# Performance work log

Hardware: AMD Instinct MI355X
Metric: run time of the kernel (lower is better)

The kernel has to match this reference:

```python
import jax, jax.numpy as jnp
import numpy as np

N_NODES = 50000

def _gat_conv(x, src, dst, W, a_src, a_dst, bias, num_nodes, concat, neg_slope=0.2):
    # x: [N, Fin]; W: [Fin, H*C]; a_src/a_dst: [H, C]; src/dst: [E]
    H, C = a_src.shape
    h = (x @ W).reshape(-1, H, C)                      # [N, H, C]
    alpha_s = jnp.einsum('nhc,hc->nh', h, a_src)        # [N, H]
    alpha_d = jnp.einsum('nhc,hc->nh', h, a_dst)        # [N, H]
    e = alpha_s[src] + alpha_d[dst]                     # [E, H]
    e = jax.nn.leaky_relu(e, neg_slope)
    # segment softmax over destination nodes
    m = jax.ops.segment_max(e, dst, num_segments=num_nodes)   # [N, H]
    ex = jnp.exp(e - m[dst])                                   # [E, H]
    denom = jax.ops.segment_sum(ex, dst, num_segments=num_nodes)  # [N, H]
    alpha = ex / denom[dst]                                    # [E, H]
    msg = h[src] * alpha[:, :, None]                            # [E, H, C]
    out = jax.ops.segment_sum(msg, dst, num_segments=num_nodes)  # [N, H, C]
    if concat:
        out = out.reshape(-1, H * C)
    else:
        out = out.mean(axis=1)
    return out + bias

def _add_self_loops(edge_index, num_nodes):
    loop = jnp.arange(num_nodes, dtype=edge_index.dtype)
    src = jnp.concatenate([edge_index[0], loop])
    dst = jnp.concatenate([edge_index[1], loop])
    return src, dst

def setup_inputs() -> dict:
    key = jax.random.key(0)
    ks = jax.random.split(key, 12)
    N, E = N_NODES, 800000
    in_c, hid, out_c, H = 128, 32, 64, 4
    x = jax.random.normal(ks[0], (N, in_c), dtype=jnp.float32)
    edge_index = jax.random.randint(ks[1], (2, E), 0, N, dtype=jnp.int64)
    edge_weight = jax.random.uniform(ks[2], (E,), dtype=jnp.float32)
    s1 = 1.0 / np.sqrt(in_c)
    s2 = 1.0 / np.sqrt(hid * H)
    W1 = jax.random.normal(ks[3], (in_c, H * hid), dtype=jnp.float32) * s1
    a_src1 = jax.random.normal(ks[4], (H, hid), dtype=jnp.float32) * s1
    a_dst1 = jax.random.normal(ks[5], (H, hid), dtype=jnp.float32) * s1
    b1 = jnp.zeros((H * hid,), dtype=jnp.float32)
    W2 = jax.random.normal(ks[6], (H * hid, out_c), dtype=jnp.float32) * s2
    a_src2 = jax.random.normal(ks[7], (1, out_c), dtype=jnp.float32) * s2
    a_dst2 = jax.random.normal(ks[8], (1, out_c), dtype=jnp.float32) * s2
    b2 = jnp.zeros((out_c,), dtype=jnp.float32)
    return {"x": x, "edge_index": edge_index, "edge_weight": edge_weight,
            "W1": W1, "a_src1": a_src1, "a_dst1": a_dst1, "b1": b1,
            "W2": W2, "a_src2": a_src2, "a_dst2": a_dst2, "b2": b2}

def reference(x, edge_index, edge_weight, W1, a_src1, a_dst1, b1, W2, a_src2, a_dst2, b2):
    # PyG GATConv with edge_dim unset ignores edge_weight; self-loops added by default
    N = x.shape[0]
    src, dst = _add_self_loops(edge_index, N)
    h = _gat_conv(x, src, dst, W1, a_src1, a_dst1, b1, N, concat=True)
    h = jax.nn.relu(h)
    out = _gat_conv(h, src, dst, W2, a_src2, a_dst2, b2, N, concat=False)
    return out
```

## Files before the change

kernel.cpp:

```cpp
#include <hip/hip_runtime.h>
#include <hip/hip_fp16.h>
#include <math.h>


#define NEG_SLOPE 0.2f
#define NBLKA 256
#define MAXNB 512
#define LDH 136

typedef _Float16 f16x8 __attribute__((ext_vector_type(8)));
typedef float f32x4 __attribute__((ext_vector_type(4)));

__device__ __forceinline__ float leaky(float v) { return v > 0.f ? v : NEG_SLOPE * v; }

__global__ __launch_bounds__(256) void histc_k(const int* __restrict__ ei, int E, int ET,
                                               int* __restrict__ blkpref, int NB,
                                               const float* __restrict__ W1,
                                               const float* __restrict__ W2,
                                               _Float16* __restrict__ w1t,
                                               _Float16* __restrict__ w2t) {
  __shared__ int lhist[MAXNB];
  int chunk = (ET + NBLKA - 1) / NBLKA;
  int e0 = blockIdx.x * chunk, e1 = min(ET, e0 + chunk);
  for (int b = threadIdx.x; b < NB; b += 256) lhist[b] = 0;
  __syncthreads();
  for (int e = e0 + threadIdx.x; e < e1; e += 256) {
    int d = (e < E) ? ei[E + e] : (e - E);
    atomicAdd(&lhist[d >> 7], 1);
  }
  __syncthreads();
  for (int b = threadIdx.x; b < NB; b += 256)
    blkpref[b * NBLKA + blockIdx.x] = lhist[b];
  if (blockIdx.x == 0) {
    int t = threadIdx.x;
    if (t < 128) {
      union { _Float16 h[8]; uint4 u; } buf;
      for (int k0 = 0; k0 < 128; k0 += 8) {
        #pragma unroll
        for (int u = 0; u < 8; ++u) buf.h[u] = (_Float16)W1[(k0 + u) * 128 + t];
        *(uint4*)&w1t[t * 128 + k0] = buf.u;
      }
    } else if (t < 192) {
      int n = t - 128;
      union { _Float16 h[8]; uint4 u; } buf;
      for (int k0 = 0; k0 < 128; k0 += 8) {
        #pragma unroll
        for (int u = 0; u < 8; ++u) buf.h[u] = (_Float16)W2[(k0 + u) * 64 + n];
        *(uint4*)&w2t[n * 128 + k0] = buf.u;
      }
    }
  }
}

__global__ __launch_bounds__(256) void scan_blk_k(int* __restrict__ blkpref,
                                                  int* __restrict__ bbase) {
  __shared__ int sm[NBLKA];
  int b = blockIdx.x, t = threadIdx.x;
  int v = blkpref[b * NBLKA + t];
  sm[t] = v;
  __syncthreads();
  #pragma unroll
  for (int off = 1; off < NBLKA; off <<= 1) {
    int x = (t >= off) ? sm[t - off] : 0;
    __syncthreads();
    sm[t] += x;
    __syncthreads();
  }
  blkpref[b * NBLKA + t] = sm[t] - v;
  if (t == NBLKA - 1) bbase[b] = sm[t];
}

__global__ __launch_bounds__(512) void scan_bkt_k(int* __restrict__ bbase,
                                                  int* __restrict__ lcnt,
                                                  int* __restrict__ rowptr,
                                                  int NB, int N, int ET) {
  __shared__ int sm[512];
  int t = threadIdx.x;
  int v = (t < NB) ? bbase[t] : 0;
  sm[t] = v;
  __syncthreads();
  #pragma unroll
  for (int off = 1; off < 512; off <<= 1) {
    int x = (t >= off) ? sm[t - off] : 0;
    __syncthreads();
    sm[t] += x;
    __syncthreads();
  }
  int excl = sm[t] - v;
  if (t <= NB) bbase[t] = excl;
  if (t == 0) { lcnt[0] = 0; lcnt[16] = 0; rowptr[N] = ET; }
}

__global__ __launch_bounds__(256) void passA_k(const int* __restrict__ ei, int E, int ET,
                                               const int* __restrict__ bbase,
                                               const int* __restrict__ blkpref,
                                               int* __restrict__ pairs, int NB) {
  __shared__ int lcur[MAXNB];
  int chunk = (ET + NBLKA - 1) / NBLKA;
  int e0 = blockIdx.x * chunk, e1 = min(ET, e0 + chunk);
  for (int b = threadIdx.x; b < NB; b += 256)
    lcur[b] = bbase[b] + blkpref[b * NBLKA + blockIdx.x];
  __syncthreads();
  for (int e = e0 + threadIdx.x; e < e1; e += 256) {
    int s, d;
    if (e < E) { s = ei[e]; d = ei[E + e]; } else { s = d = e - E; }
    int b = d >> 7;
    int pos = atomicAdd(&lcur[b], 1);
    pairs[pos] = ((d & 127) << 17) | s;
  }
}

__global__ __launch_bounds__(256) void passB_k(const int* __restrict__ pairs,
                                               const int* __restrict__ bbase,
                                               int* __restrict__ rowptr,
                                               int* __restrict__ srcs,
                                               int* __restrict__ small_list,
                                               int* __restrict__ big_list,
                                               int* __restrict__ lcnt, int N) {
  __shared__ int ncnt[128], spre[128], lcur[128];
  __shared__ int wcS[2], wcB[2], bS, bB;
  int b = blockIdx.x, t = threadIdx.x;
  int nb0 = b << 7;
  int nn = min(128, N - nb0);
  int e0 = bbase[b], e1 = bbase[b + 1];
  if (t < 128) ncnt[t] = 0;
  __syncthreads();
  for (int r = e0 + t; r < e1; r += 256)
    atomicAdd(&ncnt[pairs[r] >> 17], 1);
  __syncthreads();
  if (t < 128) spre[t] = ncnt[t];
  __syncthreads();
  #pragma unroll
  for (int off = 1; off < 128; off <<= 1) {
    int x = (t < 128 && t >= off) ? spre[t - off] : 0;
    __syncthreads();
    if (t < 128) spre[t] += x;
    __syncthreads();
  }
  if (t < nn) {
    int base = e0 + spre[t] - ncnt[t];
    rowptr[nb0 + t] = base;
    lcur[t] = base;
  }
  __syncthreads();
  for (int r = e0 + t; r < e1; r += 256) {
    int p = pairs[r];
    int pos = atomicAdd(&lcur[p >> 17], 1);
    srcs[pos] = p & 0x1FFFF;
  }
  int lane = t & 63, wv = t >> 6;
  bool valid = (t < nn);
  int deg = valid ? ncnt[t] : 0;
  bool isS = valid && (deg <= 16);
  bool isB = valid && (deg > 16);
  unsigned long long ms = __ballot(isS);
  unsigned long long mb = __ballot(isB);
  if (lane == 0 && wv < 2) { wcS[wv] = __popcll(ms); wcB[wv] = __popcll(mb); }
  __syncthreads();
  if (t == 0) {
    bS = atomicAdd(&lcnt[0],  wcS[0] + wcS[1]);
    bB = atomicAdd(&lcnt[16], wcB[0] + wcB[1]);
  }
  __syncthreads();
  unsigned long long below = (lane == 0) ? 0ull : (~0ull >> (64 - lane));
  int offS = bS + ((wv == 1) ? wcS[0] : 0);
  int offB = bB + ((wv == 1) ? wcB[0] : 0);
  if (isS) small_list[offS + __popcll(ms & below)] = nb0 + t;
  if (isB) big_list[offB + __popcll(mb & below)]   = nb0 + t;
}

__global__ __launch_bounds__(256) void gemm1_k(const float* __restrict__ X,
                                               const _Float16* __restrict__ WT,
                                               const float* __restrict__ aw_s,
                                               const float* __restrict__ aw_d,
                                               __half* __restrict__ Hh,
                                               float* __restrict__ as,
                                               float* __restrict__ ad, int N) {
  __shared__ _Float16 xs[64 * LDH];
  __shared__ _Float16 wt[128 * LDH];
  int t = threadIdx.x;
  int n0 = blockIdx.x * 64;
  for (int i = t; i < 2048; i += 256) {
    int r = i >> 4, c8 = i & 15;
    *(uint4*)&wt[r * LDH + c8 * 8] = ((const uint4*)WT)[i];
  }
  for (int i = t; i < 2048; i += 256) {
    int r = i >> 5, c4 = i & 31;
    int n = n0 + r;
    float4 xv = (n < N) ? ((const float4*)X)[(size_t)n * 32 + c4]
                        : make_float4(0.f, 0.f, 0.f, 0.f);
    __half2 h0 = __floats2half2_rn(xv.x, xv.y);
    __half2 h1 = __floats2half2_rn(xv.z, xv.w);
    uint2 u; u.x = *(unsigned*)&h0; u.y = *(unsigned*)&h1;
    *(uint2*)&xs[r * LDH + c4 * 4] = u;
  }
  __syncthreads();
  int wv = t >> 6, l = t & 63;
  int row16 = l & 15, kg = l >> 4;
  f32x4 acc[8];
  #pragma unroll
  for (int j = 0; j < 8; ++j) acc[j] = (f32x4){0.f, 0.f, 0.f, 0.f};
  #pragma unroll
  for (int kk = 0; kk < 4; ++kk) {
    int kbase = kk * 32 + kg * 8;
    f16x8 afr = *(f16x8*)&xs[(wv * 16 + row16) * LDH + kbase];
    #pragma unroll
    for (int j = 0; j < 8; ++j) {
      f16x8 bfr = *(f16x8*)&wt[(j * 16 + row16) * LDH + kbase];
      acc[j] = __builtin_amdgcn_mfma_f32_16x16x32_f16(afr, bfr, acc[j], 0, 0, 0);
    }
  }
  __syncthreads();
  #pragma unroll
  for (int j = 0; j < 8; ++j) {
    int col = j * 16 + row16;
    #pragma unroll
    for (int r = 0; r < 4; ++r) {
      int row = wv * 16 + kg * 4 + r;
      xs[row * LDH + col] = (_Float16)acc[j][r];
    }
  }
  __syncthreads();
  for (int i = t; i < 1024; i += 256) {
    int r = i >> 4, c8 = i & 15;
    int n = n0 + r;
    if (n < N) ((uint4*)Hh)[(size_t)n * 16 + c8] = *(uint4*)&xs[r * LDH + c8 * 8];
  }
  {
    int r = t >> 2, h = t & 3;
    int n = n0 + r;
    float ps = 0.f, pd = 0.f;
    #pragma unroll
    for (int q = 0; q < 4; ++q) {
      f16x8 hv = *(f16x8*)&xs[r * LDH + h * 32 + q * 8];
      float4 s0 = *(const float4*)&aw_s[h * 32 + q * 8];
      float4 s1 = *(const float4*)&aw_s[h * 32 + q * 8 + 4];
      float4 d0 = *(const float4*)&aw_d[h * 32 + q * 8];
      float4 d1 = *(const float4*)&aw_d[h * 32 + q * 8 + 4];
      ps += (float)hv[0] * s0.x + (float)hv[1] * s0.y + (float)hv[2] * s0.z + (float)hv[3] * s0.w
          + (float)hv[4] * s1.x + (float)hv[5] * s1.y + (float)hv[6] * s1.z + (float)hv[7] * s1.w;
      pd += (float)hv[0] * d0.x + (float)hv[1] * d0.y + (float)hv[2] * d0.z + (float)hv[3] * d0.w
          + (float)hv[4] * d1.x + (float)hv[5] * d1.y + (float)hv[6] * d1.z + (float)hv[7] * d1.w;
    }
    if (n < N) { as[n * 4 + h] = ps; ad[n * 4 + h] = pd; }
  }
}

__global__ __launch_bounds__(256) void gemm2_k(const __half* __restrict__ X,
                                               const _Float16* __restrict__ WT,
                                               const float* __restrict__ aw_s,
                                               const float* __restrict__ aw_d,
                                               __half* __restrict__ Hh,
                                               float* __restrict__ as,
                                               float* __restrict__ ad, int N) {
  __shared__ _Float16 xs[64 * LDH];
  __shared__ _Float16 wt[64 * LDH];
  int t = threadIdx.x;
  int n0 = blockIdx.x * 64;
  for (int i = t; i < 1024; i += 256) {
    int r = i >> 4, c8 = i & 15;
    *(uint4*)&wt[r * LDH + c8 * 8] = ((const uint4*)WT)[i];
  }
  for (int i = t; i < 1024; i += 256) {
    int r = i >> 4, c8 = i & 15;
    int n = n0 + r;
    uint4 v = (n < N) ? ((const uint4*)X)[(size_t)n * 16 + c8] : make_uint4(0, 0, 0, 0);
    *(uint4*)&xs[r * LDH + c8 * 8] = v;
  }
  __syncthreads();
  int wv = t >> 6, l = t & 63;
  int row16 = l & 15, kg = l >> 4;
  f32x4 acc[4];
  #pragma unroll
  for (int j = 0; j < 4; ++j) acc[j] = (f32x4){0.f, 0.f, 0.f, 0.f};
  #pragma unroll
  for (int kk = 0; kk < 4; ++kk) {
    int kbase = kk * 32 + kg * 8;
    f16x8 afr = *(f16x8*)&xs[(wv * 16 + row16) * LDH + kbase];
    #pragma unroll
    for (int j = 0; j < 4; ++j) {
      f16x8 bfr = *(f16x8*)&wt[(j * 16 + row16) * LDH + kbase];
      acc[j] = __builtin_amdgcn_mfma_f32_16x16x32_f16(afr, bfr, acc[j], 0, 0, 0);
    }
  }
  __syncthreads();
  #pragma unroll
  for (int j = 0; j < 4; ++j) {
    int col = j * 16 + row16;
    #pragma unroll
    for (int r = 0; r < 4; ++r) {
      int row = wv * 16 + kg * 4 + r;
      xs[row * LDH + col] = (_Float16)acc[j][r];
    }
  }
  __syncthreads();
  for (int i = t; i < 512; i += 256) {
    int r = i >> 3, c8 = i & 7;
    int n = n0 + r;
    if (n < N) ((uint4*)Hh)[(size_t)n * 8 + c8] = *(uint4*)&xs[r * LDH + c8 * 8];
  }
  {
    int r = t >> 2, q = t & 3;
    int n = n0 + r;
    float ps = 0.f, pd = 0.f;
    #pragma unroll
    for (int qq = 0; qq < 2; ++qq) {
      f16x8 hv = *(f16x8*)&xs[r * LDH + q * 16 + qq * 8];
      float4 s0 = *(const float4*)&aw_s[q * 16 + qq * 8];
      float4 s1 = *(const float4*)&aw_s[q * 16 + qq * 8 + 4];
      float4 d0 = *(const float4*)&aw_d[q * 16 + qq * 8];
      float4 d1 = *(const float4*)&aw_d[q * 16 + qq * 8 + 4];
      ps += (float)hv[0] * s0.x + (float)hv[1] * s0.y + (float)hv[2] * s0.z + (float)hv[3] * s0.w
          + (float)hv[4] * s1.x + (float)hv[5] * s1.y + (float)hv[6] * s1.z + (float)hv[7] * s1.w;
      pd += (float)hv[0] * d0.x + (float)hv[1] * d0.y + (float)hv[2] * d0.z + (float)hv[3] * d0.w
          + (float)hv[4] * d1.x + (float)hv[5] * d1.y + (float)hv[6] * d1.z + (float)hv[7] * d1.w;
    }
    ps += __shfl_xor(ps, 1); ps += __shfl_xor(ps, 2);
    pd += __shfl_xor(pd, 1); pd += __shfl_xor(pd, 2);
    if (q == 0 && n < N) { as[n] = ps; ad[n] = pd; }
  }
}

__device__ __forceinline__ void load8h(const __half* p, float* f) {
  uint4 hv = *(const uint4*)p;
  float2 f0 = __half22float2(*(const __half2*)&hv.x);
  float2 f1 = __half22float2(*(const __half2*)&hv.y);
  float2 f2 = __half22float2(*(const __half2*)&hv.z);
  float2 f3 = __half22float2(*(const __half2*)&hv.w);
  f[0] = f0.x; f[1] = f0.y; f[2] = f1.x; f[3] = f1.y;
  f[4] = f2.x; f[5] = f2.y; f[6] = f3.x; f[7] = f3.y;
}

__global__ __launch_bounds__(256) void agg1_k(const int* __restrict__ rowptr,
                                              const int* __restrict__ srcs,
                                              const float* __restrict__ as,
                                              const float* __restrict__ ad,
                                              const __half* __restrict__ Hm,
                                              const float* __restrict__ bias,
                                              __half* __restrict__ out,
                                              const int* __restrict__ small_list,
                                              const int* __restrict__ big_list,
                                              const int* __restrict__ lcnt, int SB) {
  if (blockIdx.x < (unsigned)SB) {
    __shared__ float al_sm[16][17][4];
    __shared__ int   sr_sm[16][16];
    int g  = threadIdx.x >> 4;
    int gl = threadIdx.x & 15;
    int gidx = blockIdx.x * 16 + g;
    if (gidx >= lcnt[0]) return;
    int n = small_list[gidx];
    int r0 = rowptr[n];
    int deg = rowptr[n + 1] - r0;
    float4 adn = *(const float4*)&ad[n * 4];

    float e0 = -INFINITY, e1 = -INFINITY, e2 = -INFINITY, e3 = -INFINITY;
    int s = 0;
    if (gl < deg) {
      s = srcs[r0 + gl];
      float4 av = *(const float4*)&as[s * 4];
      e0 = leaky(av.x + adn.x); e1 = leaky(av.y + adn.y);
      e2 = leaky(av.z + adn.z); e3 = leaky(av.w + adn.w);
    }
    sr_sm[g][gl] = s;
    float m0 = e0, m1 = e1, m2 = e2, m3 = e3;
    #pragma unroll
    for (int off = 8; off > 0; off >>= 1) {
      m0 = fmaxf(m0, __shfl_xor(m0, off, 16)); m1 = fmaxf(m1, __shfl_xor(m1, off, 16));
      m2 = fmaxf(m2, __shfl_xor(m2, off, 16)); m3 = fmaxf(m3, __shfl_xor(m3, off, 16));
    }
    float sc0 = (gl < deg) ? __expf(e0 - m0) : 0.f;
    float sc1 = (gl < deg) ? __expf(e1 - m1) : 0.f;
    float sc2 = (gl < deg) ? __expf(e2 - m2) : 0.f;
    float sc3 = (gl < deg) ? __expf(e3 - m3) : 0.f;
    float s0 = sc0, s1 = sc1, s2 = sc2, s3 = sc3;
    #pragma unroll
    for (int off = 8; off > 0; off >>= 1) {
      s0 += __shfl_xor(s0, off, 16); s1 += __shfl_xor(s1, off, 16);
      s2 += __shfl_xor(s2, off, 16); s3 += __shfl_xor(s3, off, 16);
    }
    *(float4*)&al_sm[g][gl][0] =
        make_float4(sc0 / s0, sc1 / s1, sc2 / s2, sc3 / s3);

    int h = gl >> 2;
    int cbase = gl * 8;
    float a0 = 0.f, a1 = 0.f, a2 = 0.f, a3 = 0.f,
          a4 = 0.f, a5 = 0.f, a6 = 0.f, a7 = 0.f;
    for (int j = 0; j < deg; j += 4) {
      #pragma unroll
      for (int u = 0; u < 4; ++u) {
        int idx = j + u;
        bool vU = idx < deg;
        int jj = vU ? idx : 0;
        int   sU  = sr_sm[g][jj];
        float alU = vU ? al_sm[g][jj][h] : 0.f;
        float f[8];
        load8h(&Hm[(size_t)sU * 128 + cbase], f);
        a0 += f[0] * alU; a1 += f[1] * alU; a2 += f[2] * alU; a3 += f[3] * alU;
        a4 += f[4] * alU; a5 += f[5] * alU; a6 += f[6] * alU; a7 += f[7] * alU;
      }
    }
    float4 b0 = *(const float4*)&bias[cbase];
    float4 b1 = *(const float4*)&bias[cbase + 4];
    __half2* dst = (__half2*)&out[(size_t)n * 128 + cbase];
    dst[0] = __floats2half2_rn(fmaxf(a0 + b0.x, 0.f), fmaxf(a1 + b0.y, 0.f));
    dst[1] = __floats2half2_rn(fmaxf(a2 + b0.z, 0.f), fmaxf(a3 + b0.w, 0.f));
    dst[2] = __floats2half2_rn(fmaxf(a4 + b1.x, 0.f), fmaxf(a5 + b1.y, 0.f));
    dst[3] = __floats2half2_rn(fmaxf(a6 + b1.z, 0.f), fmaxf(a7 + b1.w, 0.f));
    return;
  }
  __shared__ float al_sm[4][64][4];
  __shared__ int   sr_sm[4][64];
  int wv = threadIdx.x >> 6, lane = threadIdx.x & 63;
  int widx = (blockIdx.x - SB) * 4 + wv;
  if (widx >= lcnt[16]) return;
  int n = big_list[widx];
  int r0 = rowptr[n], r1 = rowptr[n + 1];
  int deg = r1 - r0;
  int grp = lane >> 4, gl = lane & 15, h = gl >> 2;
  int cbase = gl * 8;
  float4 adn = *(const float4*)&ad[n * 4];

  float a0 = 0.f, a1 = 0.f, a2 = 0.f, a3 = 0.f,
        a4 = 0.f, a5 = 0.f, a6 = 0.f, a7 = 0.f;

  if (deg <= 64) {
    float e0 = -INFINITY, e1 = -INFINITY, e2 = -INFINITY, e3 = -INFINITY;
    int s = 0;
    if (lane < deg) {
      s = srcs[r0 + lane];
      float4 av = *(const float4*)&as[s * 4];
      e0 = leaky(av.x + adn.x); e1 = leaky(av.y + adn.y);
      e2 = leaky(av.z + adn.z); e3 = leaky(av.w + adn.w);
    }
    sr_sm[wv][lane] = s;
    float m0 = e0, m1 = e1, m2 = e2, m3 = e3;
    #pragma unroll
    for (int off = 32; off > 0; off >>= 1) {
      m0 = fmaxf(m0, __shfl_xor(m0, off)); m1 = fmaxf(m1, __shfl_xor(m1, off));
      m2 = fmaxf(m2, __shfl_xor(m2, off)); m3 = fmaxf(m3, __shfl_xor(m3, off));
    }
    float sc0 = (lane < deg) ? __expf(e0 - m0) : 0.f;
    float sc1 = (lane < deg) ? __expf(e1 - m1) : 0.f;
    float sc2 = (lane < deg) ? __expf(e2 - m2) : 0.f;
    float sc3 = (lane < deg) ? __expf(e3 - m3) : 0.f;
    float s0 = sc0, s1 = sc1, s2 = sc2, s3 = sc3;
    #pragma unroll
    for (int off = 32; off > 0; off >>= 1) {
      s0 += __shfl_xor(s0, off); s1 += __shfl_xor(s1, off);
      s2 += __shfl_xor(s2, off); s3 += __shfl_xor(s3, off);
    }
    *(float4*)&al_sm[wv][lane][0] =
        make_float4(sc0 / s0, sc1 / s1, sc2 / s2, sc3 / s3);

    for (int base = 0; base < deg; base += 16) {
      #pragma unroll
      for (int u = 0; u < 4; ++u) {
        int idx = base + grp * 4 + u;
        bool vU = idx < deg;
        int jj = vU ? idx : 0;
        int   sU  = sr_sm[wv][jj];
        float alU = vU ? al_sm[wv][jj][h] : 0.f;
        float f[8];
        load8h(&Hm[(size_t)sU * 128 + cbase], f);
        a0 += f[0] * alU; a1 += f[1] * alU; a2 += f[2] * alU; a3 += f[3] * alU;
        a4 += f[4] * alU; a5 += f[5] * alU; a6 += f[6] * alU; a7 += f[7] * alU;
      }
    }
  } else {
    float m0 = -INFINITY, m1 = -INFINITY, m2 = -INFINITY, m3 = -INFINITY;
    for (int r = r0 + lane; r < r1; r += 64) {
      int s = srcs[r];
      float4 av = *(const float4*)&as[s * 4];
      m0 = fmaxf(m0, leaky(av.x + adn.x)); m1 = fmaxf(m1, leaky(av.y + adn.y));
      m2 = fmaxf(m2, leaky(av.z + adn.z)); m3 = fmaxf(m3, leaky(av.w + adn.w));
    }
    #pragma unroll
    for (int off = 32; off > 0; off >>= 1) {
      m0 = fmaxf(m0, __shfl_xor(m0, off)); m1 = fmaxf(m1, __shfl_xor(m1, off));
      m2 = fmaxf(m2, __shfl_xor(m2, off)); m3 = fmaxf(m3, __shfl_xor(m3, off));
    }
    float s0 = 0.f, s1 = 0.f, s2 = 0.f, s3 = 0.f;
    for (int r = r0 + lane; r < r1; r += 64) {
      int s = srcs[r];
      float4 av = *(const float4*)&as[s * 4];
      s0 += __expf(leaky(av.x + adn.x) - m0); s1 += __expf(leaky(av.y + adn.y) - m1);
      s2 += __expf(leaky(av.z + adn.z) - m2); s3 += __expf(leaky(av.w + adn.w) - m3);
    }
    #pragma unroll
    for (int off = 32; off > 0; off >>= 1) {
      s0 += __shfl_xor(s0, off); s1 += __shfl_xor(s1, off);
      s2 += __shfl_xor(s2, off); s3 += __shfl_xor(s3, off);
    }
    float mhh = (h == 0) ? m0 : (h == 1) ? m1 : (h == 2) ? m2 : m3;
    float inv = 1.f / ((h == 0) ? s0 : (h == 1) ? s1 : (h == 2) ? s2 : s3);
    float adh = (h == 0) ? adn.x : (h == 1) ? adn.y : (h == 2) ? adn.z : adn.w;
    for (int r = r0; r < r1; r += 8) {
      int rA = r + grp, rB = rA + 4;
      bool vA = rA < r1, vB = rB < r1;
      int sA = srcs[vA ? rA : r0];
      int sB = srcs[vB ? rB : r0];
      float avA = as[sA * 4 + h], avB = as[sB * 4 + h];
      float alA = vA ? (__expf(leaky(avA + adh) - mhh) * inv) : 0.f;
      float alB = vB ? (__expf(leaky(avB + adh) - mhh) * inv) : 0.f;
      float fA[8], fB[8];
      load8h(&Hm[(size_t)sA * 128 + cbase], fA);
      load8h(&Hm[(size_t)sB * 128 + cbase], fB);
      a0 += fA[0] * alA + fB[0] * alB; a1 += fA[1] * alA + fB[1] * alB;
      a2 += fA[2] * alA + fB[2] * alB; a3 += fA[3] * alA + fB[3] * alB;
      a4 += fA[4] * alA + fB[4] * alB; a5 += fA[5] * alA + fB[5] * alB;
      a6 += fA[6] * alA + fB[6] * alB; a7 += fA[7] * alA + fB[7] * alB;
    }
  }
  a0 += __shfl_xor(a0, 16); a0 += __shfl_xor(a0, 32);
  a1 += __shfl_xor(a1, 16); a1 += __shfl_xor(a1, 32);
  a2 += __shfl_xor(a2, 16); a2 += __shfl_xor(a2, 32);
  a3 += __shfl_xor(a3, 16); a3 += __shfl_xor(a3, 32);
  a4 += __shfl_xor(a4, 16); a4 += __shfl_xor(a4, 32);
  a5 += __shfl_xor(a5, 16); a5 += __shfl_xor(a5, 32);
  a6 += __shfl_xor(a6, 16); a6 += __shfl_xor(a6, 32);
  a7 += __shfl_xor(a7, 16); a7 += __shfl_xor(a7, 32);
  if (grp == 0) {
    float4 b0 = *(const float4*)&bias[cbase];
    float4 b1 = *(const float4*)&bias[cbase + 4];
    __half2* dst = (__half2*)&out[(size_t)n * 128 + cbase];
    dst[0] = __floats2half2_rn(fmaxf(a0 + b0.x, 0.f), fmaxf(a1 + b0.y, 0.f));
    dst[1] = __floats2half2_rn(fmaxf(a2 + b0.z, 0.f), fmaxf(a3 + b0.w, 0.f));
    dst[2] = __floats2half2_rn(fmaxf(a4 + b1.x, 0.f), fmaxf(a5 + b1.y, 0.f));
    dst[3] = __floats2half2_rn(fmaxf(a6 + b1.z, 0.f), fmaxf(a7 + b1.w, 0.f));
  }
}

__global__ __launch_bounds__(256) void agg2_k(const int* __restrict__ rowptr,
                                              const int* __restrict__ srcs,
                                              const float* __restrict__ as,
                                              const float* __restrict__ ad,
                                              const __half* __restrict__ Hm,
                                              const float* __restrict__ bias,
                                              float* __restrict__ out,
                                              const int* __restrict__ small_list,
                                              const int* __restrict__ big_list,
                                              const int* __restrict__ lcnt, int SB) {
  if (blockIdx.x < (unsigned)SB) {
    __shared__ float al_sm[16][17];
    __shared__ int   sr_sm[16][16];
    int g  = threadIdx.x >> 4;
    int gl = threadIdx.x & 15;
    int gidx = blockIdx.x * 16 + g;
    if (gidx >= lcnt[0]) return;
    int n = small_list[gidx];
    int r0 = rowptr[n];
    int deg = rowptr[n + 1] - r0;
    float adn = ad[n];

    float e = -INFINITY;
    int s = 0;
    if (gl < deg) { s = srcs[r0 + gl]; e = leaky(as[s] + adn); }
    sr_sm[g][gl] = s;
    float m = e;
    #pragma unroll
    for (int off = 8; off > 0; off >>= 1) m = fmaxf(m, __shfl_xor(m, off, 16));
    float sc = (gl < deg) ? __expf(e - m) : 0.f;
    float ssum = sc;
    #pragma unroll
    for (int off = 8; off > 0; off >>= 1) ssum += __shfl_xor(ssum, off, 16);
    al_sm[g][gl] = sc / ssum;

    int cbase = gl * 4;
    float a0 = 0.f, a1 = 0.f, a2 = 0.f, a3 = 0.f;
    for (int j = 0; j < deg; j += 4) {
      #pragma unroll
      for (int u = 0; u < 4; ++u) {
        int idx = j + u;
        bool vU = idx < deg;
        int jj = vU ? idx : 0;
        int   sU  = sr_sm[g][jj];
        float alU = vU ? al_sm[g][jj] : 0.f;
        uint2 hv = *(const uint2*)&Hm[(size_t)sU * 64 + cbase];
        float2 f0 = __half22float2(*(const __half2*)&hv.x);
        float2 f1 = __half22float2(*(const __half2*)&hv.y);
        a0 += f0.x * alU; a1 += f0.y * alU; a2 += f1.x * alU; a3 += f1.y * alU;
      }
    }
    float4 bv = *(const float4*)&bias[cbase];
    float4 o;
    o.x = a0 + bv.x; o.y = a1 + bv.y; o.z = a2 + bv.z; o.w = a3 + bv.w;
    *(float4*)&out[(size_t)n * 64 + cbase] = o;
    return;
  }
  __shared__ float al_sm[4][64];
  __shared__ int   sr_sm[4][64];
  int wv = threadIdx.x >> 6, lane = threadIdx.x & 63;
  int widx = (blockIdx.x - SB) * 4 + wv;
  if (widx >= lcnt[16]) return;
  int n = big_list[widx];
  int r0 = rowptr[n], r1 = rowptr[n + 1];
  int deg = r1 - r0;
  int grp = lane >> 4, gl = lane & 15;
  int cbase = gl * 4;
  float adn = ad[n];

  float a0 = 0.f, a1 = 0.f, a2 = 0.f, a3 = 0.f;

  if (deg <= 64) {
    float e = -INFINITY;
    int s = 0;
    if (lane < deg) { s = srcs[r0 + lane]; e = leaky(as[s] + adn); }
    sr_sm[wv][lane] = s;
    float m = e;
    #pragma unroll
    for (int off = 32; off > 0; off >>= 1) m = fmaxf(m, __shfl_xor(m, off));
    float sc = (lane < deg) ? __expf(e - m) : 0.f;
    float ssum = sc;
    #pragma unroll
    for (int off = 32; off > 0; off >>= 1) ssum += __shfl_xor(ssum, off);
    al_sm[wv][lane] = sc / ssum;

    for (int base = 0; base < deg; base += 16) {
      #pragma unroll
      for (int u = 0; u < 4; ++u) {
        int idx = base + grp * 4 + u;
        bool vU = idx < deg;
        int jj = vU ? idx : 0;
        int   sU  = sr_sm[wv][jj];
        float alU = vU ? al_sm[wv][jj] : 0.f;
        uint2 hv = *(const uint2*)&Hm[(size_t)sU * 64 + cbase];
        float2 f0 = __half22float2(*(const __half2*)&hv.x);
        float2 f1 = __half22float2(*(const __half2*)&hv.y);
        a0 += f0.x * alU; a1 += f0.y * alU; a2 += f1.x * alU; a3 += f1.y * alU;
      }
    }
  } else {
    float mh = -INFINITY;
    for (int r = r0 + lane; r < r1; r += 64)
      mh = fmaxf(mh, leaky(as[srcs[r]] + adn));
    #pragma unroll
    for (int off = 32; off > 0; off >>= 1) mh = fmaxf(mh, __shfl_xor(mh, off));
    float ssum = 0.f;
    for (int r = r0 + lane; r < r1; r += 64)
      ssum += __expf(leaky(as[srcs[r]] + adn) - mh);
    #pragma unroll
    for (int off = 32; off > 0; off >>= 1) ssum += __shfl_xor(ssum, off);
    float inv = 1.f / ssum;
    for (int r = r0; r < r1; r += 8) {
      int rA = r + grp, rB = rA + 4;
      bool vA = rA < r1, vB = rB < r1;
      int sA = srcs[vA ? rA : r0];
      int sB = srcs[vB ? rB : r0];
      float alA = vA ? (__expf(leaky(as[sA] + adn) - mh) * inv) : 0.f;
      float alB = vB ? (__expf(leaky(as[sB] + adn) - mh) * inv) : 0.f;
      uint2 hvA = *(const uint2*)&Hm[(size_t)sA * 64 + cbase];
      uint2 hvB = *(const uint2*)&Hm[(size_t)sB * 64 + cbase];
      float2 fA0 = __half22float2(*(const __half2*)&hvA.x);
      float2 fA1 = __half22float2(*(const __half2*)&hvA.y);
      float2 fB0 = __half22float2(*(const __half2*)&hvB.x);
      float2 fB1 = __half22float2(*(const __half2*)&hvB.y);
      a0 += fA0.x * alA + fB0.x * alB; a1 += fA0.y * alA + fB0.y * alB;
      a2 += fA1.x * alA + fB1.x * alB; a3 += fA1.y * alA + fB1.y * alB;
    }
  }
  a0 += __shfl_xor(a0, 16); a0 += __shfl_xor(a0, 32);
  a1 += __shfl_xor(a1, 16); a1 += __shfl_xor(a1, 32);
  a2 += __shfl_xor(a2, 16); a2 += __shfl_xor(a2, 32);
  a3 += __shfl_xor(a3, 16); a3 += __shfl_xor(a3, 32);
  if (grp == 0) {
    float4 bv = *(const float4*)&bias[cbase];
    float4 o;
    o.x = a0 + bv.x; o.y = a1 + bv.y; o.z = a2 + bv.z; o.w = a3 + bv.w;
    *(float4*)&out[(size_t)n * 64 + cbase] = o;
  }
}

extern "C" void kernel_launch(void* const* d_in, const int* in_sizes, int n_in,
                              void* d_out, int out_size, void* d_ws, size_t ws_size,
                              hipStream_t stream) {
  const float* x   = (const float*)d_in[0];
  const int*   ei  = (const int*)d_in[1];
  const float* W1  = (const float*)d_in[3];
  const float* aS1 = (const float*)d_in[4];
  const float* aD1 = (const float*)d_in[5];
  const float* b1  = (const float*)d_in[6];
  const float* W2  = (const float*)d_in[7];
  const float* aS2 = (const float*)d_in[8];
  const float* aD2 = (const float*)d_in[9];
  const float* b2  = (const float*)d_in[10];

  const int N  = in_sizes[0] / 128;
  const int E  = in_sizes[2];
  const int ET = E + N;
  const int NB = (N + 127) >> 7;

  float* ws    = (float*)d_ws;
  __half* h1h  = (__half*)ws;
  __half* o1h  = (__half*)(ws + (size_t)N * 64);
  float* as1   = ws + (size_t)N * 128;
  float* ad1   = as1  + (size_t)4 * N;
  float* as2   = ad1  + (size_t)4 * N;
  float* ad2   = as2  + (size_t)N;
  int*   lcnt    = (int*)(ad2 + (size_t)N);
  int*   rowptr  = lcnt + 32;
  int*   bbase   = rowptr + N + 1;
  int*   blkpref = bbase + NB + 1;
  int*   small_list = blkpref + NB * NBLKA;
  int*   big_list   = small_list + N;
  int*   srcs   = big_list + N;
  _Float16* w1t = (_Float16*)(srcs + ET);
  _Float16* w2t = w1t + 128 * 128;
  int*   pairs  = (int*)ws;
  __half* h2h  = h1h;
  float* out  = (float*)d_out;

  const int gb = (N + 63) / 64;
  const int sb = (N + 15) / 16;
  const int bb = (N + 3) / 4;

  histc_k<<<NBLKA, 256, 0, stream>>>(ei, E, ET, blkpref, NB, W1, W2, w1t, w2t);
  scan_blk_k<<<NB, 256, 0, stream>>>(blkpref, bbase);
  scan_bkt_k<<<1, 512, 0, stream>>>(bbase, lcnt, rowptr, NB, N, ET);
  passA_k<<<NBLKA, 256, 0, stream>>>(ei, E, ET, bbase, blkpref, pairs, NB);
  passB_k<<<NB, 256, 0, stream>>>(pairs, bbase, rowptr, srcs,
                                  small_list, big_list, lcnt, N);

  gemm1_k<<<gb, 256, 0, stream>>>(x, w1t, aS1, aD1, h1h, as1, ad1, N);
  agg1_k<<<sb + bb, 256, 0, stream>>>(rowptr, srcs, as1, ad1, h1h, b1, o1h,
                                      small_list, big_list, lcnt, sb);

  gemm2_k<<<gb, 256, 0, stream>>>(o1h, w2t, aS2, aD2, h2h, as2, ad2, N);
  agg2_k<<<sb + bb, 256, 0, stream>>>(rowptr, srcs, as2, ad2, h2h, b2, out,
                                      small_list, big_list, lcnt, sb);
}
```

Measured before the change: 216.4 us.

## Fuse bucket scan into block scan, use nontemporal memory ops, unroll gathers

Removes the single-block scan_bkt_k launch by having the last-finishing scan_blk_k block (detected with an atomic counter reset in histc_k) perform the bucket-level prefix scan. Many global loads and stores across the CSR build, GEMM and aggregation kernels become nontemporal hints, and the small-degree aggregation loops unroll by 8 instead of 4. This saves one kernel launch and aims to reduce cache pollution from streaming data. The cost is more register pressure from the wider unroll, and nontemporal hints may hurt data such as srcs that is reread by the second aggregation pass.

```diff
diff --git a/kernel.cpp b/kernel.cpp
--- a/kernel.cpp
+++ b/kernel.cpp
@@ -10,6 +10,7 @@
 
 typedef _Float16 f16x8 __attribute__((ext_vector_type(8)));
 typedef float f32x4 __attribute__((ext_vector_type(4)));
+typedef unsigned int u32x4 __attribute__((ext_vector_type(4)));
 
 __device__ __forceinline__ float leaky(float v) { return v > 0.f ? v : NEG_SLOPE * v; }
 
@@ -18,14 +19,15 @@
                                                const float* __restrict__ W1,
                                                const float* __restrict__ W2,
                                                _Float16* __restrict__ w1t,
-                                               _Float16* __restrict__ w2t) {
+                                               _Float16* __restrict__ w2t,
+                                               int* __restrict__ lcnt) {
   __shared__ int lhist[MAXNB];
   int chunk = (ET + NBLKA - 1) / NBLKA;
   int e0 = blockIdx.x * chunk, e1 = min(ET, e0 + chunk);
   for (int b = threadIdx.x; b < NB; b += 256) lhist[b] = 0;
   __syncthreads();
   for (int e = e0 + threadIdx.x; e < e1; e += 256) {
-    int d = (e < E) ? ei[E + e] : (e - E);
+    int d = (e < E) ? __builtin_nontemporal_load(&ei[E + e]) : (e - E);
     atomicAdd(&lhist[d >> 7], 1);
   }
   __syncthreads();
@@ -33,28 +35,33 @@
     blkpref[b * NBLKA + blockIdx.x] = lhist[b];
   if (blockIdx.x == 0) {
     int t = threadIdx.x;
+    if (t == 255) lcnt[31] = 0;
     if (t < 128) {
-      union { _Float16 h[8]; uint4 u; } buf;
+      union { _Float16 h[8]; u32x4 u; } buf;
       for (int k0 = 0; k0 < 128; k0 += 8) {
         #pragma unroll
         for (int u = 0; u < 8; ++u) buf.h[u] = (_Float16)W1[(k0 + u) * 128 + t];
-        *(uint4*)&w1t[t * 128 + k0] = buf.u;
+        *(u32x4*)&w1t[t * 128 + k0] = buf.u;
       }
     } else if (t < 192) {
       int n = t - 128;
-      union { _Float16 h[8]; uint4 u; } buf;
+      union { _Float16 h[8]; u32x4 u; } buf;
       for (int k0 = 0; k0 < 128; k0 += 8) {
         #pragma unroll
         for (int u = 0; u < 8; ++u) buf.h[u] = (_Float16)W2[(k0 + u) * 64 + n];
-        *(uint4*)&w2t[n * 128 + k0] = buf.u;
+        *(u32x4*)&w2t[n * 128 + k0] = buf.u;
       }
     }
   }
 }
 
 __global__ __launch_bounds__(256) void scan_blk_k(int* __restrict__ blkpref,
-                                                  int* __restrict__ bbase) {
+                                                  int* __restrict__ bbase,
+                                                  int* __restrict__ lcnt,
+                                                  int* __restrict__ rowptr,
+                                                  int NB, int N, int ET) {
   __shared__ int sm[NBLKA];
+  __shared__ int lastflag;
   int b = blockIdx.x, t = threadIdx.x;
   int v = blkpref[b * NBLKA + t];
   sm[t] = v;
@@ -68,26 +75,26 @@
   }
   blkpref[b * NBLKA + t] = sm[t] - v;
   if (t == NBLKA - 1) bbase[b] = sm[t];
-}
-
-__global__ __launch_bounds__(512) void scan_bkt_k(int* __restrict__ bbase,
-                                                  int* __restrict__ lcnt,
-                                                  int* __restrict__ rowptr,
-                                                  int NB, int N, int ET) {
-  __shared__ int sm[512];
-  int t = threadIdx.x;
-  int v = (t < NB) ? bbase[t] : 0;
-  sm[t] = v;
-  __syncthreads();
-  #pragma unroll
-  for (int off = 1; off < 512; off <<= 1) {
+  __threadfence();
+  if (t == 0) lastflag = atomicAdd(&lcnt[31], 1);
+  __syncthreads();
+  if (lastflag != (int)gridDim.x - 1) return;
+  int i0 = 2 * t, i1 = 2 * t + 1;
+  int a = (i0 < NB) ? atomicAdd(&bbase[i0], 0) : 0;
+  int c = (i1 < NB) ? atomicAdd(&bbase[i1], 0) : 0;
+  __syncthreads();
+  sm[t] = a + c;
+  __syncthreads();
+  #pragma unroll
+  for (int off = 1; off < 256; off <<= 1) {
     int x = (t >= off) ? sm[t - off] : 0;
     __syncthreads();
     sm[t] += x;
     __syncthreads();
   }
-  int excl = sm[t] - v;
-  if (t <= NB) bbase[t] = excl;
+  int base = sm[t] - (a + c);
+  if (i0 <= NB) bbase[i0] = base;
+  if (i1 <= NB) bbase[i1] = base + a;
   if (t == 0) { lcnt[0] = 0; lcnt[16] = 0; rowptr[N] = ET; }
 }
 
@@ -103,10 +110,13 @@
   __syncthreads();
   for (int e = e0 + threadIdx.x; e < e1; e += 256) {
     int s, d;
-    if (e < E) { s = ei[e]; d = ei[E + e]; } else { s = d = e - E; }
+    if (e < E) {
+      s = __builtin_nontemporal_load(&ei[e]);
+      d = __builtin_nontemporal_load(&ei[E + e]);
+    } else { s = d = e - E; }
     int b = d >> 7;
     int pos = atomicAdd(&lcur[b], 1);
-    pairs[pos] = ((d & 127) << 17) | s;
+    __builtin_nontemporal_store(((d & 127) << 17) | s, &pairs[pos]);
   }
 }
 
@@ -146,7 +156,7 @@
   for (int r = e0 + t; r < e1; r += 256) {
     int p = pairs[r];
     int pos = atomicAdd(&lcur[p >> 17], 1);
-    srcs[pos] = p & 0x1FFFF;
+    __builtin_nontemporal_store(p & 0x1FFFF, &srcs[pos]);
   }
   int lane = t & 63, wv = t >> 6;
   bool valid = (t < nn);
@@ -182,15 +192,15 @@
   int n0 = blockIdx.x * 64;
   for (int i = t; i < 2048; i += 256) {
     int r = i >> 4, c8 = i & 15;
-    *(uint4*)&wt[r * LDH + c8 * 8] = ((const uint4*)WT)[i];
+    *(u32x4*)&wt[r * LDH + c8 * 8] = ((const u32x4*)WT)[i];
   }
   for (int i = t; i < 2048; i += 256) {
     int r = i >> 5, c4 = i & 31;
     int n = n0 + r;
-    float4 xv = (n < N) ? ((const float4*)X)[(size_t)n * 32 + c4]
-                        : make_float4(0.f, 0.f, 0.f, 0.f);
-    __half2 h0 = __floats2half2_rn(xv.x, xv.y);
-    __half2 h1 = __floats2half2_rn(xv.z, xv.w);
+    f32x4 xv = (n < N) ? __builtin_nontemporal_load(&((const f32x4*)X)[(size_t)n * 32 + c4])
+                       : (f32x4){0.f, 0.f, 0.f, 0.f};
+    __half2 h0 = __floats2half2_rn(xv[0], xv[1]);
+    __half2 h1 = __floats2half2_rn(xv[2], xv[3]);
     uint2 u; u.x = *(unsigned*)&h0; u.y = *(unsigned*)&h1;
     *(uint2*)&xs[r * LDH + c4 * 4] = u;
   }
@@ -224,7 +234,9 @@
   for (int i = t; i < 1024; i += 256) {
     int r = i >> 4, c8 = i & 15;
     int n = n0 + r;
-    if (n < N) ((uint4*)Hh)[(size_t)n * 16 + c8] = *(uint4*)&xs[r * LDH + c8 * 8];
+    if (n < N)
+      __builtin_nontemporal_store(*(u32x4*)&xs[r * LDH + c8 * 8],
+                                  &((u32x4*)Hh)[(size_t)n * 16 + c8]);
   }
   {
     int r = t >> 2, h = t & 3;
@@ -259,13 +271,14 @@
   int n0 = blockIdx.x * 64;
   for (int i = t; i < 1024; i += 256) {
     int r = i >> 4, c8 = i & 15;
-    *(uint4*)&wt[r * LDH + c8 * 8] = ((const uint4*)WT)[i];
+    *(u32x4*)&wt[r * LDH + c8 * 8] = ((const u32x4*)WT)[i];
   }
   for (int i = t; i < 1024; i += 256) {
     int r = i >> 4, c8 = i & 15;
     int n = n0 + r;
-    uint4 v = (n < N) ? ((const uint4*)X)[(size_t)n * 16 + c8] : make_uint4(0, 0, 0, 0);
-    *(uint4*)&xs[r * LDH + c8 * 8] = v;
+    u32x4 v = (n < N) ? __builtin_nontemporal_load(&((const u32x4*)X)[(size_t)n * 16 + c8])
+                      : (u32x4){0, 0, 0, 0};
+    *(u32x4*)&xs[r * LDH + c8 * 8] = v;
   }
   __syncthreads();
   int wv = t >> 6, l = t & 63;
@@ -297,7 +310,9 @@
   for (int i = t; i < 512; i += 256) {
     int r = i >> 3, c8 = i & 7;
     int n = n0 + r;
-    if (n < N) ((uint4*)Hh)[(size_t)n * 8 + c8] = *(uint4*)&xs[r * LDH + c8 * 8];
+    if (n < N)
+      __builtin_nontemporal_store(*(u32x4*)&xs[r * LDH + c8 * 8],
+                                  &((u32x4*)Hh)[(size_t)n * 8 + c8]);
   }
   {
     int r = t >> 2, q = t & 3;
@@ -356,7 +371,7 @@
     float e0 = -INFINITY, e1 = -INFINITY, e2 = -INFINITY, e3 = -INFINITY;
     int s = 0;
     if (gl < deg) {
-      s = srcs[r0 + gl];
+      s = __builtin_nontemporal_load(&srcs[r0 + gl]);
       float4 av = *(const float4*)&as[s * 4];
       e0 = leaky(av.x + adn.x); e1 = leaky(av.y + adn.y);
       e2 = leaky(av.z + adn.z); e3 = leaky(av.w + adn.w);
@@ -385,9 +400,9 @@
     int cbase = gl * 8;
     float a0 = 0.f, a1 = 0.f, a2 = 0.f, a3 = 0.f,
           a4 = 0.f, a5 = 0.f, a6 = 0.f, a7 = 0.f;
-    for (int j = 0; j < deg; j += 4) {
+    for (int j = 0; j < deg; j += 8) {
       #pragma unroll
-      for (int u = 0; u < 4; ++u) {
+      for (int u = 0; u < 8; ++u) {
         int idx = j + u;
         bool vU = idx < deg;
         int jj = vU ? idx : 0;
@@ -401,11 +416,12 @@
     }
     float4 b0 = *(const float4*)&bias[cbase];
     float4 b1 = *(const float4*)&bias[cbase + 4];
-    __half2* dst = (__half2*)&out[(size_t)n * 128 + cbase];
-    dst[0] = __floats2half2_rn(fmaxf(a0 + b0.x, 0.f), fmaxf(a1 + b0.y, 0.f));
-    dst[1] = __floats2half2_rn(fmaxf(a2 + b0.z, 0.f), fmaxf(a3 + b0.w, 0.f));
-    dst[2] = __floats2half2_rn(fmaxf(a4 + b1.x, 0.f), fmaxf(a5 + b1.y, 0.f));
-    dst[3] = __floats2half2_rn(fmaxf(a6 + b1.z, 0.f), fmaxf(a7 + b1.w, 0.f));
+    union { __half2 h2[4]; u32x4 u; } ov;
+    ov.h2[0] = __floats2half2_rn(fmaxf(a0 + b0.x, 0.f), fmaxf(a1 + b0.y, 0.f));
+    ov.h2[1] = __floats2half2_rn(fmaxf(a2 + b0.z, 0.f), fmaxf(a3 + b0.w, 0.f));
+    ov.h2[2] = __floats2half2_rn(fmaxf(a4 + b1.x, 0.f), fmaxf(a5 + b1.y, 0.f));
+    ov.h2[3] = __floats2half2_rn(fmaxf(a6 + b1.z, 0.f), fmaxf(a7 + b1.w, 0.f));
+    __builtin_nontemporal_store(ov.u, (u32x4*)&out[(size_t)n * 128 + cbase]);
     return;
   }
   __shared__ float al_sm[4][64][4];
@@ -427,7 +443,7 @@
     float e0 = -INFINITY, e1 = -INFINITY, e2 = -INFINITY, e3 = -INFINITY;
     int s = 0;
     if (lane < deg) {
-      s = srcs[r0 + lane];
+      s = __builtin_nontemporal_load(&srcs[r0 + lane]);
       float4 av = *(const float4*)&as[s * 4];
       e0 = leaky(av.x + adn.x); e1 = leaky(av.y + adn.y);
       e2 = leaky(av.z + adn.z); e3 = leaky(av.w + adn.w);
@@ -522,11 +538,12 @@
   if (grp == 0) {
     float4 b0 = *(const float4*)&bias[cbase];
     float4 b1 = *(const float4*)&bias[cbase + 4];
-    __half2* dst = (__half2*)&out[(size_t)n * 128 + cbase];
-    dst[0] = __floats2half2_rn(fmaxf(a0 + b0.x, 0.f), fmaxf(a1 + b0.y, 0.f));
-    dst[1] = __floats2half2_rn(fmaxf(a2 + b0.z, 0.f), fmaxf(a3 + b0.w, 0.f));
-    dst[2] = __floats2half2_rn(fmaxf(a4 + b1.x, 0.f), fmaxf(a5 + b1.y, 0.f));
-    dst[3] = __floats2half2_rn(fmaxf(a6 + b1.z, 0.f), fmaxf(a7 + b1.w, 0.f));
+    union { __half2 h2[4]; u32x4 u; } ov;
+    ov.h2[0] = __floats2half2_rn(fmaxf(a0 + b0.x, 0.f), fmaxf(a1 + b0.y, 0.f));
+    ov.h2[1] = __floats2half2_rn(fmaxf(a2 + b0.z, 0.f), fmaxf(a3 + b0.w, 0.f));
+    ov.h2[2] = __floats2half2_rn(fmaxf(a4 + b1.x, 0.f), fmaxf(a5 + b1.y, 0.f));
+    ov.h2[3] = __floats2half2_rn(fmaxf(a6 + b1.z, 0.f), fmaxf(a7 + b1.w, 0.f));
+    __builtin_nontemporal_store(ov.u, (u32x4*)&out[(size_t)n * 128 + cbase]);
   }
 }
 
@@ -554,7 +571,7 @@
 
     float e = -INFINITY;
     int s = 0;
-    if (gl < deg) { s = srcs[r0 + gl]; e = leaky(as[s] + adn); }
+    if (gl < deg) { s = __builtin_nontemporal_load(&srcs[r0 + gl]); e = leaky(as[s] + adn); }
     sr_sm[g][gl] = s;
     float m = e;
     #pragma unroll
@@ -567,9 +584,9 @@
 
     int cbase = gl * 4;
     float a0 = 0.f, a1 = 0.f, a2 = 0.f, a3 = 0.f;
-    for (int j = 0; j < deg; j += 4) {
+    for (int j = 0; j < deg; j += 8) {
       #pragma unroll
-      for (int u = 0; u < 4; ++u) {
+      for (int u = 0; u < 8; ++u) {
         int idx = j + u;
         bool vU = idx < deg;
         int jj = vU ? idx : 0;
@@ -582,9 +599,9 @@
       }
     }
     float4 bv = *(const float4*)&bias[cbase];
-    float4 o;
-    o.x = a0 + bv.x; o.y = a1 + bv.y; o.z = a2 + bv.z; o.w = a3 + bv.w;
-    *(float4*)&out[(size_t)n * 64 + cbase] = o;
+    f32x4 o;
+    o[0] = a0 + bv.x; o[1] = a1 + bv.y; o[2] = a2 + bv.z; o[3] = a3 + bv.w;
+    __builtin_nontemporal_store(o, (f32x4*)&out[(size_t)n * 64 + cbase]);
     return;
   }
   __shared__ float al_sm[4][64];
@@ -604,7 +621,7 @@
   if (deg <= 64) {
     float e = -INFINITY;
     int s = 0;
-    if (lane < deg) { s = srcs[r0 + lane]; e = leaky(as[s] + adn); }
+    if (lane < deg) { s = __builtin_nontemporal_load(&srcs[r0 + lane]); e = leaky(as[s] + adn); }
     sr_sm[wv][lane] = s;
     float m = e;
     #pragma unroll
@@ -664,9 +681,9 @@
   a3 += __shfl_xor(a3, 16); a3 += __shfl_xor(a3, 32);
   if (grp == 0) {
     float4 bv = *(const float4*)&bias[cbase];
-    float4 o;
-    o.x = a0 + bv.x; o.y = a1 + bv.y; o.z = a2 + bv.z; o.w = a3 + bv.w;
-    *(float4*)&out[(size_t)n * 64 + cbase] = o;
+    f32x4 o;
+    o[0] = a0 + bv.x; o[1] = a1 + bv.y; o[2] = a2 + bv.z; o[3] = a3 + bv.w;
+    __builtin_nontemporal_store(o, (f32x4*)&out[(size_t)n * 64 + cbase]);
   }
 }
 
@@ -713,9 +730,8 @@
   const int sb = (N + 15) / 16;
   const int bb = (N + 3) / 4;
 
-  histc_k<<<NBLKA, 256, 0, stream>>>(ei, E, ET, blkpref, NB, W1, W2, w1t, w2t);
-  scan_blk_k<<<NB, 256, 0, stream>>>(blkpref, bbase);
-  scan_bkt_k<<<1, 512, 0, stream>>>(bbase, lcnt, rowptr, NB, N, ET);
+  histc_k<<<NBLKA, 256, 0, stream>>>(ei, E, ET, blkpref, NB, W1, W2, w1t, w2t, lcnt);
+  scan_blk_k<<<NB, 256, 0, stream>>>(blkpref, bbase, lcnt, rowptr, NB, N, ET);
   passA_k<<<NBLKA, 256, 0, stream>>>(ei, E, ET, bbase, blkpref, pairs, NB);
   passB_k<<<NB, 256, 0, stream>>>(pairs, bbase, rowptr, srcs,
                                   small_list, big_list, lcnt, N);
```

Result: slower. 258.0 us (+19.2%).
